# Kernel tuning notes

Hardware: AMD Instinct MI355X
Metric: run time of the kernel (lower is better)

## Reference

```python
import jax, jax.numpy as jnp
import numpy as np

N = 50000   # nodes
E = 800000  # edges (avg degree 16)
D = 256     # input = hidden = output dim
L = 3       # num_layers


def setup_inputs() -> dict:
    key = jax.random.key(0)
    k0, k1, k2, k3 = jax.random.split(key, 4)
    x = jax.random.normal(k0, (N, D), dtype=jnp.float32)
    edge_index = jax.random.randint(k1, (2, E), 0, N, dtype=jnp.int32)
    # SAGEConv params per layer: lin_l (neighbor path, with bias), lin_r (root path)
    Wl = jax.random.normal(k2, (L, D, D), dtype=jnp.float32) * 0.05
    Wr = jax.random.normal(k3, (L, D, D), dtype=jnp.float32) * 0.05
    b = jnp.zeros((L, D), dtype=jnp.float32)
    return {"x": x, "edge_index": edge_index, "Wl": Wl, "Wr": Wr, "b": b}


def reference(x, edge_index, Wl, Wr, b):
    src = edge_index[0]
    dst = edge_index[1]
    # in-degree for mean aggregation (clamped to avoid div-by-zero)
    deg = jax.ops.segment_sum(jnp.ones((E,), x.dtype), dst, num_segments=N)
    inv_deg = (1.0 / jnp.maximum(deg, 1.0))[:, None]  # [N,1]
    h = x
    for i in range(L):
        # gather source features, scatter-add into destinations, then mean
        agg = jax.ops.segment_sum(h[src], dst, num_segments=N) * inv_deg  # [N,D]
        h = agg @ Wl[i] + h @ Wr[i] + b[i]
        if i < L - 1:
            h = jax.nn.relu(h)  # dropout(p=0.1) is identity in eval mode
    return h
```

## Files before the change

### kernel.cpp

```cpp
#include <hip/hip_runtime.h>


typedef __attribute__((ext_vector_type(8))) _Float16 f16x8;
typedef __attribute__((ext_vector_type(4))) float f32x4;

__global__ void count_deg_kernel(const int* __restrict__ dst,
                                 int* __restrict__ deg, int E) {
    int i = (blockIdx.x * blockDim.x + threadIdx.x) * 2;
    if (i + 1 < E) {
        int2 d = *(const int2*)&dst[i];
        atomicAdd(&deg[d.x], 1);
        atomicAdd(&deg[d.y], 1);
    } else if (i < E) {
        atomicAdd(&deg[dst[i]], 1);
    }
}

__device__ __forceinline__ int block_excl_scan_256(int v, int tid) {
    int lane = tid & 63, w = tid >> 6;
    int x = v;
#pragma unroll
    for (int off = 1; off < 64; off <<= 1) {
        int y = __shfl_up(x, off);
        if (lane >= off) x += y;
    }
    __shared__ int wsum[4], woff[4];
    if (lane == 63) wsum[w] = x;
    __syncthreads();
    if (tid == 0) {
        int a = 0;
#pragma unroll
        for (int i = 0; i < 4; ++i) { woff[i] = a; a += wsum[i]; }
    }
    __syncthreads();
    return woff[w] + x - v;
}

__global__ void scan_phase1(const int* __restrict__ deg,
                            int* __restrict__ partial, int n) {
    int base = blockIdx.x * 1024;
    int s = 0;
    for (int i = threadIdx.x; i < 1024; i += 256) {
        int idx = base + i;
        s += (idx < n) ? deg[idx] : 0;
    }
    __shared__ int ws4[4];
    int lane = threadIdx.x & 63, w = threadIdx.x >> 6;
#pragma unroll
    for (int off = 32; off; off >>= 1) s += __shfl_down(s, off);
    if (lane == 0) ws4[w] = s;
    __syncthreads();
    if (threadIdx.x == 0)
        partial[blockIdx.x] = ws4[0] + ws4[1] + ws4[2] + ws4[3];
}

__global__ void scan_phase2(int* __restrict__ partial, int nb,
                            int* __restrict__ rowptr, int n, int E) {
    int tid = threadIdx.x;
    int v = (tid < nb) ? partial[tid] : 0;
    int ex = block_excl_scan_256(v, tid);
    if (tid < nb) partial[tid] = ex;
    if (tid == 0) rowptr[n] = E;
}

__global__ void scan_phase3(const int* __restrict__ deg,
                            const int* __restrict__ partial,
                            int* __restrict__ rowptr, int* __restrict__ cursor,
                            float* __restrict__ inv_deg, int n) {
    int base = blockIdx.x * 1024 + threadIdx.x * 4;
    int d[4];
#pragma unroll
    for (int j = 0; j < 4; ++j) {
        int idx = base + j;
        d[j] = (idx < n) ? deg[idx] : 0;
    }
    int tsum = d[0] + d[1] + d[2] + d[3];
    int ex = block_excl_scan_256(tsum, threadIdx.x);
    int run = partial[blockIdx.x] + ex;
#pragma unroll
    for (int j = 0; j < 4; ++j) {
        int idx = base + j;
        if (idx < n) {
            rowptr[idx] = run;
            cursor[idx] = run;
            inv_deg[idx] = 1.0f / (float)max(d[j], 1);
        }
        run += d[j];
    }
}

__global__ void fill_csr_xcd_kernel(const int* __restrict__ src,
                                    const int* __restrict__ dst,
                                    int* __restrict__ cursor,
                                    int* __restrict__ csr_src, int E, int n) {
    const int g = blockIdx.x & 7;
    const int lo = g * (n >> 3);
    const int hi = (g == 7) ? n : lo + (n >> 3);
    int i = ((blockIdx.x >> 3) * 256 + threadIdx.x) * 2;
    if (i + 1 < E) {
        int2 d = *(const int2*)&dst[i];
        if ((d.x >= lo && d.x < hi) || (d.y >= lo && d.y < hi)) {
            int2 s = *(const int2*)&src[i];
            if (d.x >= lo && d.x < hi) {
                int p = atomicAdd(&cursor[d.x], 1);
                csr_src[p] = s.x;
            }
            if (d.y >= lo && d.y < hi) {
                int p = atomicAdd(&cursor[d.y], 1);
                csr_src[p] = s.y;
            }
        }
    } else if (i < E) {
        int d = dst[i];
        if (d >= lo && d < hi) {
            int p = atomicAdd(&cursor[d], 1);
            csr_src[p] = src[i];
        }
    }
}

__global__ void presplit_w_kernel(const float* __restrict__ Wl,
                                  const float* __restrict__ Wr,
                                  _Float16* __restrict__ Wf,
                                  int* __restrict__ deg, int N, int total) {
    int idx = blockIdx.x * blockDim.x + threadIdx.x;
    if (idx < N) deg[idx] = 0;
    if (idx >= total) return;
    int l = idx >> 17;
    int rem = idx & 131071;
    int s = rem >> 16;
    int kc = rem & 65535;
    int k = kc >> 8, c = kc & 255;
    const float* W = s ? Wr : Wl;
    float w = W[((size_t)l * 256 + k) * 256 + c];
    int k0c = k >> 5, g = (k >> 3) & 3, j = k & 7;
    int tile = c >> 4, col = c & 15;
    int fi = (l * 2 + s) * 65536 + k0c * 8192 + ((tile * 4 + g) * 16 + col) * 8 + j;
    Wf[fi] = (_Float16)w;
}

__global__ __launch_bounds__(512) void gemm_dual_kernel(
    const float* __restrict__ xsrc, const _Float16* __restrict__ hsrc,
    int f32src, _Float16* __restrict__ zl, _Float16* __restrict__ zr,
    const _Float16* __restrict__ Wf_l, const float* __restrict__ bias, int M) {
    __shared__ __align__(16) _Float16 Ah[32][65][8];
    const int tid = threadIdx.x;
    const int r0 = blockIdx.x * 64;
    const int wave = tid >> 6, lane = tid & 63;
    const int l15 = lane & 15, lg = lane >> 4;
    const int wr = (wave & 1) * 32;
    const int wc = (wave >> 1) * 64;
    const int tg0 = wc >> 4;
    const _Float16* wbase = Wf_l + (lg * 16 + l15) * 8;

    f16x8 blc[4], brc[4];
#pragma unroll
    for (int t = 0; t < 4; ++t) {
        blc[t] = *(const f16x8*)&wbase[(tg0 + t) * 512];
        brc[t] = *(const f16x8*)&wbase[65536 + (tg0 + t) * 512];
    }

#pragma unroll
    for (int i = 0; i < 4; ++i) {
        int idx = i * 512 + tid;
        int row = idx >> 5, g = idx & 31;
        int grow = r0 + row;
        f16x8 v = (f16x8)(_Float16)0;
        if (grow < M) {
            if (f32src) {
                const float4* p =
                    (const float4*)&xsrc[(size_t)grow * 256 + g * 8];
                float4 v0 = p[0], v1 = p[1];
                v[0] = (_Float16)v0.x; v[1] = (_Float16)v0.y;
                v[2] = (_Float16)v0.z; v[3] = (_Float16)v0.w;
                v[4] = (_Float16)v1.x; v[5] = (_Float16)v1.y;
                v[6] = (_Float16)v1.z; v[7] = (_Float16)v1.w;
            } else {
                int p = g >> 2, off = (g & 3) * 8;
                v = *(const f16x8*)&hsrc[((size_t)p * M + grow) * 32 + off];
            }
        }
        *(f16x8*)&Ah[g][row][0] = v;
    }
    __syncthreads();

    f32x4 accl[2][4], accr[2][4];
#pragma unroll
    for (int rt = 0; rt < 2; ++rt)
#pragma unroll
        for (int t = 0; t < 4; ++t) {
            accl[rt][t] = (f32x4)(0.0f);
            accr[rt][t] = (f32x4)(0.0f);
        }

#pragma unroll
    for (int s = 0; s < 8; ++s) {
        f16x8 bln[4], brn[4];
        if (s < 7) {
            const _Float16* wn = wbase + (s + 1) * 8192;
#pragma unroll
            for (int t = 0; t < 4; ++t) {
                bln[t] = *(const f16x8*)&wn[(tg0 + t) * 512];
                brn[t] = *(const f16x8*)&wn[65536 + (tg0 + t) * 512];
            }
        }
        f16x8 a0 = *(const f16x8*)&Ah[s * 4 + lg][wr + l15][0];
        f16x8 a1 = *(const f16x8*)&Ah[s * 4 + lg][wr + 16 + l15][0];
#pragma unroll
        for (int t = 0; t < 4; ++t) {
            accl[0][t] = __builtin_amdgcn_mfma_f32_16x16x32_f16(a0, blc[t],
                                                                accl[0][t], 0, 0, 0);
            accl[1][t] = __builtin_amdgcn_mfma_f32_16x16x32_f16(a1, blc[t],
                                                                accl[1][t], 0, 0, 0);
            accr[0][t] = __builtin_amdgcn_mfma_f32_16x16x32_f16(a0, brc[t],
                                                                accr[0][t], 0, 0, 0);
            accr[1][t] = __builtin_amdgcn_mfma_f32_16x16x32_f16(a1, brc[t],
                                                                accr[1][t], 0, 0, 0);
        }
        if (s < 7) {
#pragma unroll
            for (int t = 0; t < 4; ++t) {
                blc[t] = bln[t];
                brc[t] = brn[t];
            }
        }
    }

    float bv[4];
#pragma unroll
    for (int t = 0; t < 4; ++t) bv[t] = bias[wc + t * 16 + l15];
#pragma unroll
    for (int rt = 0; rt < 2; ++rt) {
#pragma unroll
        for (int r = 0; r < 4; ++r) {
            int grow = r0 + wr + rt * 16 + lg * 4 + r;
            if (grow >= M) continue;
#pragma unroll
            for (int t = 0; t < 4; ++t) {
                int col = wc + t * 16 + l15;
                int p = col >> 5, off = col & 31;
                size_t zi = ((size_t)p * M + grow) * 32 + off;
                zl[zi] = (_Float16)accl[rt][t][r];
                zr[zi] = (_Float16)(accr[rt][t][r] + bv[t]);
            }
        }
    }
}

__global__ __launch_bounds__(256) void combine_panel_kernel(
    const _Float16* __restrict__ zl, const _Float16* __restrict__ zr,
    const int* __restrict__ rowptr, const int* __restrict__ csr_src,
    const float* __restrict__ inv_deg, _Float16* __restrict__ hout,
    float* __restrict__ fout, int n, int mode) {
    const int slice = blockIdx.x & 7;
    const int chunk = blockIdx.x >> 3;
    const int grp = threadIdx.x >> 3;
    const int sub = threadIdx.x & 7;
    const int pair = sub >> 2;
    const int l4 = sub & 3;
    const _Float16* zlp = zl + (size_t)slice * n * 32 + l4 * 8;
    const _Float16* zrp = zr + (size_t)slice * n * 32 + l4 * 8;

    int v = chunk * 32 + grp;
    if (v >= n) return;
    int beg = rowptr[v], end = rowptr[v + 1];
    float sc = inv_deg[v];
    float o[8];
    if (beg < end) {
        f16x8 acc0 = (f16x8)(_Float16)0, acc1 = (f16x8)(_Float16)0;
        for (int e = beg; e < end; e += 16) {
            int e0 = e + pair * 8;
            f16x8 t[8];
#pragma unroll
            for (int k = 0; k < 8; ++k) {
                int ee = min(e0 + k, end - 1);
                int u = csr_src[ee];
                t[k] = *(const f16x8*)&zlp[(size_t)u * 32];
            }
#pragma unroll
            for (int k = 0; k < 4; ++k) {
                acc0 += t[k];
                acc1 += t[k + 4];
            }
        }
        int d = end - beg;
        int T = (d + 15) >> 4;
        int rem = d - ((T - 1) << 4);
        int valid = pair ? max(rem - 8, 0) : min(rem, 8);
        float inval = (float)(8 - valid);
        int ulast = csr_src[end - 1];
        f16x8 tl = *(const f16x8*)&zlp[(size_t)ulast * 32];
#pragma unroll
        for (int j = 0; j < 8; ++j)
            o[j] = (float)acc0[j] + (float)acc1[j] - inval * (float)tl[j];
    } else {
#pragma unroll
        for (int j = 0; j < 8; ++j) o[j] = 0.0f;
    }
#pragma unroll
    for (int j = 0; j < 8; ++j) o[j] += __shfl_xor(o[j], 4);
    if (pair == 0) {
        f16x8 zp = *(const f16x8*)&zrp[(size_t)v * 32];
#pragma unroll
        for (int j = 0; j < 8; ++j) o[j] = o[j] * sc + (float)zp[j];
        if (mode == 0) {
            f16x8 hv;
#pragma unroll
            for (int j = 0; j < 8; ++j) hv[j] = (_Float16)fmaxf(o[j], 0.0f);
            *(f16x8*)&hout[((size_t)slice * n + v) * 32 + l4 * 8] = hv;
        } else {
            int cbase = slice * 32 + l4 * 8;
            float4* op = (float4*)&fout[(size_t)v * 256 + cbase];
            op[0] = make_float4(o[0], o[1], o[2], o[3]);
            op[1] = make_float4(o[4], o[5], o[6], o[7]);
        }
    }
}

extern "C" void kernel_launch(void* const* d_in, const int* in_sizes, int n_in,
                              void* d_out, int out_size, void* d_ws, size_t ws_size,
                              hipStream_t stream) {
    const int D = 256;
    const int N = in_sizes[0] / D;
    const int E = in_sizes[1] / 2;
    const int L = in_sizes[2] / (D * D);

    const float* x  = (const float*)d_in[0];
    const int*   ei = (const int*)d_in[1];
    const float* Wl = (const float*)d_in[2];
    const float* Wr = (const float*)d_in[3];
    const float* b  = (const float*)d_in[4];
    const int* src = ei;
    const int* dst = ei + E;

    size_t off = 0;
    auto alloc = [&](size_t bytes) {
        void* p = (char*)d_ws + off;
        off += (bytes + 255) & ~(size_t)255;
        return p;
    };
    int*   deg     = (int*)alloc((size_t)N * 4);
    int*   rowptr  = (int*)alloc((size_t)(N + 1) * 4);
    int*   cursor  = (int*)alloc((size_t)N * 4);
    float* inv_deg = (float*)alloc((size_t)N * 4);
    int*   csr_src = (int*)alloc((size_t)E * 4);
    int*   partial = (int*)alloc(256 * 4);
    _Float16* zlP  = (_Float16*)alloc((size_t)N * D * 2);
    _Float16* zrP  = (_Float16*)alloc((size_t)N * D * 2);
    _Float16* hbuf = (_Float16*)alloc((size_t)N * D * 2);
    _Float16* Wf   = (_Float16*)alloc((size_t)L * 2 * 65536 * 2);
    (void)ws_size;

    _Float16* zlQ = (_Float16*)d_out;
    _Float16* zrQ = zlQ + (size_t)N * D;
    float* outf = (float*)d_out;

    const int scan_blocks = (N + 1023) / 1024;

    int wtotal = L * 2 * 65536;
    hipLaunchKernelGGL(presplit_w_kernel, dim3((wtotal + 255) / 256), dim3(256),
                       0, stream, Wl, Wr, Wf, deg, N, wtotal);

    hipLaunchKernelGGL(count_deg_kernel, dim3((E / 2 + 255) / 256), dim3(256),
                       0, stream, dst, deg, E);
    hipLaunchKernelGGL(scan_phase1, dim3(scan_blocks), dim3(256), 0, stream,
                       deg, partial, N);
    hipLaunchKernelGGL(scan_phase2, dim3(1), dim3(256), 0, stream,
                       partial, scan_blocks, rowptr, N, E);
    hipLaunchKernelGGL(scan_phase3, dim3(scan_blocks), dim3(256), 0, stream,
                       deg, partial, rowptr, cursor, inv_deg, N);
    const int fill_chunks = (E / 2 + 255) / 256;
    hipLaunchKernelGGL(fill_csr_xcd_kernel, dim3(8 * fill_chunks), dim3(256),
                       0, stream, src, dst, cursor, csr_src, E, N);

    const int gemm_blocks = (N + 63) / 64;
    const int comb_blocks = 8 * ((N + 31) / 32);

    hipLaunchKernelGGL(gemm_dual_kernel, dim3(gemm_blocks), dim3(512), 0,
                       stream, x, (const _Float16*)nullptr, 1, zlP, zrP,
                       Wf, b, N);
    hipLaunchKernelGGL(combine_panel_kernel, dim3(comb_blocks), dim3(256), 0,
                       stream, zlP, zrP, rowptr, csr_src, inv_deg,
                       hbuf, outf, N, 0);
    hipLaunchKernelGGL(gemm_dual_kernel, dim3(gemm_blocks), dim3(512), 0,
                       stream, (const float*)nullptr, hbuf, 0, zlQ, zrQ,
                       Wf + 131072, b + D, N);
    hipLaunchKernelGGL(combine_panel_kernel, dim3(comb_blocks), dim3(256), 0,
                       stream, zlQ, zrQ, rowptr, csr_src, inv_deg,
                       hbuf, outf, N, 0);
    hipLaunchKernelGGL(gemm_dual_kernel, dim3(gemm_blocks), dim3(512), 0,
                       stream, (const float*)nullptr, hbuf, 0, zlP, zrP,
                       Wf + 262144, b + 2 * D, N);
    hipLaunchKernelGGL(combine_panel_kernel, dim3(comb_blocks), dim3(256), 0,
                       stream, zlP, zrP, rowptr, csr_src, inv_deg,
                       hbuf, outf, N, 1);
}
```

Before: 343.4 us.

## Sort nodes by degree trip-class to balance combine kernel warps

```diff
diff --git a/kernel.cpp b/kernel.cpp
--- a/kernel.cpp
+++ b/kernel.cpp
@@ -117,6 +117,57 @@
             csr_src[p] = src[i];
         }
     }
+}
+
+__device__ __forceinline__ int trip_class(int d) {
+    return min((d + 15) >> 4, 3);
+}
+
+__global__ void class_hist_kernel(const int* __restrict__ deg,
+                                  int* __restrict__ ccnt, int n, int nb) {
+    __shared__ int h[4];
+    if (threadIdx.x < 4) h[threadIdx.x] = 0;
+    __syncthreads();
+    int i = blockIdx.x * 256 + threadIdx.x;
+    if (i < n) atomicAdd(&h[trip_class(deg[i])], 1);
+    __syncthreads();
+    if (threadIdx.x < 4) ccnt[threadIdx.x * nb + blockIdx.x] = h[threadIdx.x];
+}
+
+__global__ void class_scan_kernel(int* __restrict__ ccnt, int total) {
+    __shared__ int carry;
+    if (threadIdx.x == 0) carry = 0;
+    __syncthreads();
+    for (int base = 0; base < total; base += 256) {
+        int i = base + threadIdx.x;
+        int v = (i < total) ? ccnt[i] : 0;
+        int ex = block_excl_scan_256(v, threadIdx.x);
+        if (i < total) ccnt[i] = carry + ex;
+        __syncthreads();
+        if (threadIdx.x == 255) carry += ex + v;
+        __syncthreads();
+    }
+}
+
+__global__ void class_scatter_kernel(const int* __restrict__ deg,
+                                     const int* __restrict__ ccnt,
+                                     int* __restrict__ perm, int n, int nb) {
+    int i = blockIdx.x * 256 + threadIdx.x;
+    bool valid = i < n;
+    int c = 0;
+    if (valid) c = trip_class(deg[i]);
+    int rank = 0, base = 0;
+#pragma unroll
+    for (int cc = 0; cc < 4; ++cc) {
+        int ind = (valid && c == cc) ? 1 : 0;
+        int ex = block_excl_scan_256(ind, threadIdx.x);
+        if (valid && c == cc) {
+            rank = ex;
+            base = ccnt[cc * nb + blockIdx.x];
+        }
+        __syncthreads();
+    }
+    if (valid) perm[base + rank] = i;
 }
 
 __global__ void presplit_w_kernel(const float* __restrict__ Wl,
@@ -250,8 +301,8 @@
 __global__ __launch_bounds__(256) void combine_panel_kernel(
     const _Float16* __restrict__ zl, const _Float16* __restrict__ zr,
     const int* __restrict__ rowptr, const int* __restrict__ csr_src,
-    const float* __restrict__ inv_deg, _Float16* __restrict__ hout,
-    float* __restrict__ fout, int n, int mode) {
+    const float* __restrict__ inv_deg, const int* __restrict__ perm,
+    _Float16* __restrict__ hout, float* __restrict__ fout, int n, int mode) {
     const int slice = blockIdx.x & 7;
     const int chunk = blockIdx.x >> 3;
     const int grp = threadIdx.x >> 3;
@@ -261,8 +312,9 @@
     const _Float16* zlp = zl + (size_t)slice * n * 32 + l4 * 8;
     const _Float16* zrp = zr + (size_t)slice * n * 32 + l4 * 8;
 
-    int v = chunk * 32 + grp;
-    if (v >= n) return;
+    int idx = chunk * 32 + grp;
+    if (idx >= n) return;
+    int v = perm[idx];
     int beg = rowptr[v], end = rowptr[v + 1];
     float sc = inv_deg[v];
     float o[8];
@@ -345,6 +397,9 @@
     float* inv_deg = (float*)alloc((size_t)N * 4);
     int*   csr_src = (int*)alloc((size_t)E * 4);
     int*   partial = (int*)alloc(256 * 4);
+    const int nb   = (N + 255) / 256;
+    int*   ccnt    = (int*)alloc((size_t)(4 * nb) * 4);
+    int*   perm    = (int*)alloc((size_t)N * 4);
     _Float16* zlP  = (_Float16*)alloc((size_t)N * D * 2);
     _Float16* zrP  = (_Float16*)alloc((size_t)N * D * 2);
     _Float16* hbuf = (_Float16*)alloc((size_t)N * D * 2);
@@ -373,6 +428,13 @@
     hipLaunchKernelGGL(fill_csr_xcd_kernel, dim3(8 * fill_chunks), dim3(256),
                        0, stream, src, dst, cursor, csr_src, E, N);
 
+    hipLaunchKernelGGL(class_hist_kernel, dim3(nb), dim3(256), 0, stream,
+                       deg, ccnt, N, nb);
+    hipLaunchKernelGGL(class_scan_kernel, dim3(1), dim3(256), 0, stream,
+                       ccnt, 4 * nb);
+    hipLaunchKernelGGL(class_scatter_kernel, dim3(nb), dim3(256), 0, stream,
+                       deg, ccnt, perm, N, nb);
+
     const int gemm_blocks = (N + 63) / 64;
     const int comb_blocks = 8 * ((N + 31) / 32);
 
@@ -380,18 +442,18 @@
                        stream, x, (const _Float16*)nullptr, 1, zlP, zrP,
                        Wf, b, N);
     hipLaunchKernelGGL(combine_panel_kernel, dim3(comb_blocks), dim3(256), 0,
-                       stream, zlP, zrP, rowptr, csr_src, inv_deg,
+                       stream, zlP, zrP, rowptr, csr_src, inv_deg, perm,
                        hbuf, outf, N, 0);
     hipLaunchKernelGGL(gemm_dual_kernel, dim3(gemm_blocks), dim3(512), 0,
                        stream, (const float*)nullptr, hbuf, 0, zlQ, zrQ,
                        Wf + 131072, b + D, N);
     hipLaunchKernelGGL(combine_panel_kernel, dim3(comb_blocks), dim3(256), 0,
-                       stream, zlQ, zrQ, rowptr, csr_src, inv_deg,
+                       stream, zlQ, zrQ, rowptr, csr_src, inv_deg, perm,
                        hbuf, outf, N, 0);
     hipLaunchKernelGGL(gemm_dual_kernel, dim3(gemm_blocks), dim3(512), 0,
                        stream, (const float*)nullptr, hbuf, 0, zlP, zrP,
                        Wf + 262144, b + 2 * D, N);
     hipLaunchKernelGGL(combine_panel_kernel, dim3(comb_blocks), dim3(256), 0,
-                       stream, zlP, zrP, rowptr, csr_src, inv_deg,
+                       stream, zlP, zrP, rowptr, csr_src, inv_deg, perm,
                        hbuf, outf, N, 1);
 }
```

After: 360.5 us. 5.0% more time.

## Retile GEMM waves to full rows and prefetch CSR indices in gather

Applied to the files above, without the earlier changes.

```diff
diff --git a/kernel.cpp b/kernel.cpp
--- a/kernel.cpp
+++ b/kernel.cpp
@@ -148,14 +148,13 @@
     const int r0 = blockIdx.x * 64;
     const int wave = tid >> 6, lane = tid & 63;
     const int l15 = lane & 15, lg = lane >> 4;
-    const int wr = (wave & 1) * 32;
-    const int wc = (wave >> 1) * 64;
+    const int wc = wave * 32;
     const int tg0 = wc >> 4;
     const _Float16* wbase = Wf_l + (lg * 16 + l15) * 8;
 
-    f16x8 blc[4], brc[4];
-#pragma unroll
-    for (int t = 0; t < 4; ++t) {
+    f16x8 blc[2], brc[2];
+#pragma unroll
+    for (int t = 0; t < 2; ++t) {
         blc[t] = *(const f16x8*)&wbase[(tg0 + t) * 512];
         brc[t] = *(const f16x8*)&wbase[65536 + (tg0 + t) * 512];
     }
@@ -184,59 +183,60 @@
     }
     __syncthreads();
 
-    f32x4 accl[2][4], accr[2][4];
-#pragma unroll
-    for (int rt = 0; rt < 2; ++rt)
-#pragma unroll
-        for (int t = 0; t < 4; ++t) {
+    f32x4 accl[4][2], accr[4][2];
+#pragma unroll
+    for (int rt = 0; rt < 4; ++rt)
+#pragma unroll
+        for (int t = 0; t < 2; ++t) {
             accl[rt][t] = (f32x4)(0.0f);
             accr[rt][t] = (f32x4)(0.0f);
         }
 
 #pragma unroll
     for (int s = 0; s < 8; ++s) {
-        f16x8 bln[4], brn[4];
+        f16x8 bln[2], brn[2];
         if (s < 7) {
             const _Float16* wn = wbase + (s + 1) * 8192;
 #pragma unroll
-            for (int t = 0; t < 4; ++t) {
+            for (int t = 0; t < 2; ++t) {
                 bln[t] = *(const f16x8*)&wn[(tg0 + t) * 512];
                 brn[t] = *(const f16x8*)&wn[65536 + (tg0 + t) * 512];
             }
         }
-        f16x8 a0 = *(const f16x8*)&Ah[s * 4 + lg][wr + l15][0];
-        f16x8 a1 = *(const f16x8*)&Ah[s * 4 + lg][wr + 16 + l15][0];
-#pragma unroll
-        for (int t = 0; t < 4; ++t) {
-            accl[0][t] = __builtin_amdgcn_mfma_f32_16x16x32_f16(a0, blc[t],
-                                                                accl[0][t], 0, 0, 0);
-            accl[1][t] = __builtin_amdgcn_mfma_f32_16x16x32_f16(a1, blc[t],
-                                                                accl[1][t], 0, 0, 0);
-            accr[0][t] = __builtin_amdgcn_mfma_f32_16x16x32_f16(a0, brc[t],
-                                                                accr[0][t], 0, 0, 0);
-            accr[1][t] = __builtin_amdgcn_mfma_f32_16x16x32_f16(a1, brc[t],
-                                                                accr[1][t], 0, 0, 0);
+        f16x8 a[4];
+#pragma unroll
+        for (int rt = 0; rt < 4; ++rt)
+            a[rt] = *(const f16x8*)&Ah[s * 4 + lg][rt * 16 + l15][0];
+#pragma unroll
+        for (int t = 0; t < 2; ++t) {
+#pragma unroll
+            for (int rt = 0; rt < 4; ++rt) {
+                accl[rt][t] = __builtin_amdgcn_mfma_f32_16x16x32_f16(
+                    a[rt], blc[t], accl[rt][t], 0, 0, 0);
+                accr[rt][t] = __builtin_amdgcn_mfma_f32_16x16x32_f16(
+                    a[rt], brc[t], accr[rt][t], 0, 0, 0);
+            }
         }
         if (s < 7) {
 #pragma unroll
-            for (int t = 0; t < 4; ++t) {
+            for (int t = 0; t < 2; ++t) {
                 blc[t] = bln[t];
                 brc[t] = brn[t];
             }
         }
     }
 
-    float bv[4];
-#pragma unroll
-    for (int t = 0; t < 4; ++t) bv[t] = bias[wc + t * 16 + l15];
-#pragma unroll
-    for (int rt = 0; rt < 2; ++rt) {
+    float bv[2];
+#pragma unroll
+    for (int t = 0; t < 2; ++t) bv[t] = bias[wc + t * 16 + l15];
+#pragma unroll
+    for (int rt = 0; rt < 4; ++rt) {
 #pragma unroll
         for (int r = 0; r < 4; ++r) {
-            int grow = r0 + wr + rt * 16 + lg * 4 + r;
+            int grow = r0 + rt * 16 + lg * 4 + r;
             if (grow >= M) continue;
 #pragma unroll
-            for (int t = 0; t < 4; ++t) {
+            for (int t = 0; t < 2; ++t) {
                 int col = wc + t * 16 + l15;
                 int p = col >> 5, off = col & 31;
                 size_t zi = ((size_t)p * M + grow) * 32 + off;
@@ -268,14 +268,20 @@
     float o[8];
     if (beg < end) {
         f16x8 acc0 = (f16x8)(_Float16)0, acc1 = (f16x8)(_Float16)0;
+        int u[8];
+#pragma unroll
+        for (int k = 0; k < 8; ++k)
+            u[k] = csr_src[min(beg + pair * 8 + k, end - 1)];
         for (int e = beg; e < end; e += 16) {
-            int e0 = e + pair * 8;
             f16x8 t[8];
 #pragma unroll
-            for (int k = 0; k < 8; ++k) {
-                int ee = min(e0 + k, end - 1);
-                int u = csr_src[ee];
-                t[k] = *(const f16x8*)&zlp[(size_t)u * 32];
+            for (int k = 0; k < 8; ++k)
+                t[k] = *(const f16x8*)&zlp[(size_t)u[k] * 32];
+            int e2 = e + 16;
+            if (e2 < end) {
+#pragma unroll
+                for (int k = 0; k < 8; ++k)
+                    u[k] = csr_src[min(e2 + pair * 8 + k, end - 1)];
             }
 #pragma unroll
             for (int k = 0; k < 4; ++k) {
```

After: 329.2 us, median of 2. 1.04x faster.
